# Performance work log

Measured on AMD Instinct MI355X. Metric: run time of the kernel, lower is better.

The kernel has to match this reference:

```python
import jax, jax.numpy as jnp
import numpy as np

N = 50000
E = 800000
F = 64
HID = 64
HEADS = 4
NTYPES = 3


def layer_norm(x, g, b, eps=1e-5):
    mu = x.mean(-1, keepdims=True)
    var = ((x - mu) ** 2).mean(-1, keepdims=True)
    return (x - mu) * jax.lax.rsqrt(var + eps) * g + b


def gat_conv(x, src, dst, n, W, att_src, att_dst, bias, concat):
    # PyG GATConv: per-head linear transform, additive attention, segment softmax over dst.
    H, C = att_src.shape
    xp = (x @ W).reshape(n, H, C)                       # [N,H,C]
    a_s = (xp * att_src).sum(-1)                         # [N,H]
    a_d = (xp * att_dst).sum(-1)                         # [N,H]
    e = jax.nn.leaky_relu(a_s[src] + a_d[dst], 0.2)      # [Etot,H]
    m = jax.ops.segment_max(e, dst, num_segments=n)      # stable softmax per target
    ex = jnp.exp(e - m[dst])
    denom = jax.ops.segment_sum(ex, dst, num_segments=n)
    alpha = ex / (denom[dst] + 1e-16)                    # [Etot,H]
    msg = xp[src] * alpha[:, :, None]                    # [Etot,H,C]
    out = jax.ops.segment_sum(msg, dst, num_segments=n)  # [N,H,C]
    out = out.reshape(n, H * C) if concat else out.mean(1)
    return out + bias


def setup_inputs() -> dict:
    key = jax.random.key(0)
    ks = jax.random.split(key, 12)
    f32 = jnp.float32
    return {
        'node_features': jax.random.normal(ks[0], (N, F), f32),
        'node_types': jax.random.randint(ks[1], (N,), 0, NTYPES),
        'edge_index': jax.random.randint(ks[2], (2, E), 0, N),
        'type_emb': jax.random.normal(ks[3], (NTYPES, HID), f32) * 0.02,
        'proj_W': jax.random.normal(ks[4], (F, HID), f32) / np.sqrt(F).astype(np.float32),
        'proj_b': jnp.zeros((HID,), f32),
        'W0': jax.random.normal(ks[5], (HID, HEADS * HID), f32) / np.sqrt(HID).astype(np.float32),
        'att_src0': jax.random.normal(ks[6], (HEADS, HID), f32) * 0.1,
        'att_dst0': jax.random.normal(ks[7], (HEADS, HID), f32) * 0.1,
        'bias0': jnp.zeros((HEADS * HID,), f32),
        'ln0_g': jnp.ones((HEADS * HID,), f32),
        'ln0_b': jnp.zeros((HEADS * HID,), f32),
        'W1': jax.random.normal(ks[8], (HEADS * HID, HEADS * HID), f32) / np.sqrt(HEADS * HID).astype(np.float32),
        'att_src1': jax.random.normal(ks[9], (HEADS, HID), f32) * 0.1,
        'att_dst1': jax.random.normal(ks[10], (HEADS, HID), f32) * 0.1,
        'bias1': jnp.zeros((HID,), f32),
        'ln1_g': jnp.ones((HID,), f32),
        'ln1_b': jnp.zeros((HID,), f32),
    }


def reference(node_features, node_types, edge_index, type_emb, proj_W, proj_b,
              W0, att_src0, att_dst0, bias0, ln0_g, ln0_b,
              W1, att_src1, att_dst1, bias1, ln1_g, ln1_b):
    n = node_features.shape[0]
    loop = jnp.arange(n)
    src = jnp.concatenate([edge_index[0], loop])  # add_self_loops=True (PyG default)
    dst = jnp.concatenate([edge_index[1], loop])
    # input projection + node-type embedding
    x = node_features @ proj_W + proj_b + type_emb[node_types]
    # layer 0: concat heads -> [N, HEADS*HID]
    h = gat_conv(x, src, dst, n, W0, att_src0, att_dst0, bias0, True)
    h = jax.nn.relu(layer_norm(h, ln0_g, ln0_b))  # dropout is identity in eval
    # layer 1: mean over heads -> [N, HID]; residual skipped (shape mismatch 256 vs 64)
    h2 = gat_conv(h, src, dst, n, W1, att_src1, att_dst1, bias1, False)
    h2 = jax.nn.relu(layer_norm(h2, ln1_g, ln1_b))
    return h2
```

## Files before the change

kernel.cpp:

```cpp
#include <hip/hip_runtime.h>
#include <hip/hip_bf16.h>
#include <hip/hip_fp16.h>

typedef unsigned short u16;
typedef unsigned int u32;
typedef short s16x8 __attribute__((ext_vector_type(8)));
typedef float f32x4 __attribute__((ext_vector_type(4)));

__device__ __forceinline__ float bf2f(u16 u) {
  return __uint_as_float(((u32)u) << 16);
}

__device__ __forceinline__ u16 f2b(float f) {
  __hip_bfloat16 h = __float2bfloat16(f);
  return *(u16*)&h;
}

__device__ __forceinline__ u32 packbf(float lo, float hi) {
  return (u32)f2b(lo) | ((u32)f2b(hi) << 16);
}

__device__ __forceinline__ bool sniff_bf16(const void* ones) {
  u32 w = *(const u32*)ones;
  return (w >> 16) == (w & 0xFFFFu);
}

__device__ __forceinline__ float ldf(const void* p, size_t i, bool bf) {
  return bf ? bf2f(((const u16*)p)[i]) : ((const float*)p)[i];
}

__global__ __launch_bounds__(256) void deg_count_k(const int* __restrict__ ei, int E, int N,
                                                   int* __restrict__ deg) {
  int i = blockIdx.x * 256 + threadIdx.x;
  if (i >= E + N) return;
  int d = (i < E) ? ei[E + i] : (i - E);
  atomicAdd(deg + d, 1);
}

__global__ __launch_bounds__(256) void scan_local_k(const int* __restrict__ deg,
                                                    int* __restrict__ off,
                                                    int* __restrict__ bsum, int N) {
  __shared__ int ps[256];
  int t = threadIdx.x;
  int i = blockIdx.x * 256 + t;
  int v = (i < N) ? deg[i] : 0;
  ps[t] = v;
  __syncthreads();
#pragma unroll
  for (int o = 1; o < 256; o <<= 1) {
    int u = (t >= o) ? ps[t - o] : 0;
    __syncthreads();
    ps[t] += u;
    __syncthreads();
  }
  if (i < N) off[i] = ps[t] - v;
  if (t == 255) bsum[blockIdx.x] = ps[255];
}

__global__ __launch_bounds__(256) void scan_add2_k(int* __restrict__ off,
                                                   const int* __restrict__ bsum,
                                                   int* __restrict__ cur,
                                                   int N, int Etot, int nb) {
  __shared__ int red[256];
  int t = threadIdx.x;
  int b = blockIdx.x;
  red[t] = (t < nb && t < b) ? bsum[t] : 0;
  __syncthreads();
#pragma unroll
  for (int o = 128; o > 0; o >>= 1) {
    if (t < o) red[t] += red[t + o];
    __syncthreads();
  }
  int pre = red[0];
  int i = b * 256 + t;
  if (i == 0) off[N] = Etot;
  if (i >= N) return;
  int o2 = off[i] + pre;
  off[i] = o2;
  cur[i] = o2;
}

__global__ __launch_bounds__(256) void scatter_k(const int* __restrict__ ei, int E, int N,
                                                 int* __restrict__ cur, int* __restrict__ csr) {
  int i = blockIdx.x * 256 + threadIdx.x;
  if (i >= E + N) return;
  int s, d;
  if (i < E) { s = ei[i]; d = ei[E + i]; } else { s = i - E; d = s; }
  int p = atomicAdd(cur + d, 1);
  csr[p] = s;
}

__global__ __launch_bounds__(256) void prep_k(
    const void* __restrict__ W0, const void* __restrict__ W1,
    const void* __restrict__ pW, const void* __restrict__ atts,
    const void* __restrict__ attd, const void* __restrict__ pb,
    const void* __restrict__ temb, const void* __restrict__ ones,
    u16* __restrict__ Wp0, u16* __restrict__ Wp1, u16* __restrict__ Wpp,
    u16* __restrict__ Wpe, float* __restrict__ ca) {
  bool bf = sniff_bf16(ones);
  int b = blockIdx.x;
  int t = threadIdx.x;
  if (b < 320) {
    const void* W = (b < 64) ? W0 : W1;
    u16* Wp = (b < 64) ? Wp0 : Wp1;
    int i = (b < 64 ? b : b - 64) * 256 + t;
    int j = i & 7;
    int q = (i >> 3) & 3;
    int c = (i >> 5) & 255;
    int kc = i >> 13;
    int k = kc * 32 + q * 8 + j;
    Wp[i] = f2b(ldf(W, (size_t)k * 256 + c, bf));
  } else if (b < 336) {
    int i = (b - 320) * 256 + t;
    int j = i & 7;
    int q = (i >> 3) & 3;
    int c = (i >> 5) & 63;
    int kc = i >> 11;
    int k = kc * 32 + q * 8 + j;
    Wpp[i] = f2b(ldf(pW, (size_t)k * 64 + c, bf));
  } else {
    __shared__ float va[256], vd[256];
    int h = t >> 6, k = t & 63;
    {
      float s = 0.f, d = 0.f;
      for (int c = 0; c < 64; c++) {
        float w = ldf(W0, (size_t)k * 256 + h * 64 + c, bf);
        s += w * ldf(atts, h * 64 + c, bf);
        d += w * ldf(attd, h * 64 + c, bf);
      }
      va[t] = s;
      vd[t] = d;
    }
    __syncthreads();
    {
      int i = k;
      float wa = 0.f, wd = 0.f;
      for (int kk = 0; kk < 64; kk++) {
        float wv = ldf(pW, (size_t)i * 64 + kk, bf);
        wa += wv * va[h * 64 + kk];
        wd += wv * vd[h * 64 + kk];
      }
      int kc = i >> 5, q = (i >> 3) & 3, j = i & 7;
      Wpe[((kc * 16 + h) * 4 + q) * 8 + j] = f2b(wa);
      Wpe[((kc * 16 + 4 + h) * 4 + q) * 8 + j] = f2b(wd);
    }
    Wpe[256 + t] = 0;
    Wpe[768 + t] = 0;
    if (t < 12) {
      int ty = t >> 2, hh = t & 3;
      float sa = 0.f, sd = 0.f;
      for (int kk = 0; kk < 64; kk++) {
        float bv = ldf(pb, kk, bf) + ldf(temb, ty * 64 + kk, bf);
        sa += bv * va[hh * 64 + kk];
        sd += bv * vd[hh * 64 + kk];
      }
      ca[t] = sa;
      ca[12 + t] = sd;
    }
  }
}

__global__ __launch_bounds__(256) void proj2_k(
    const void* __restrict__ nf, const int* __restrict__ ntype,
    const u16* __restrict__ Wpp, const u16* __restrict__ Wpe,
    const void* __restrict__ pbias, const void* __restrict__ temb,
    const float* __restrict__ ca, const void* __restrict__ ones,
    u16* __restrict__ x, float* __restrict__ aS, float* __restrict__ aD, int N) {
  bool bf = sniff_bf16(ones);
  int t = threadIdx.x;
  int wave = t >> 6, lane = t & 63;
  int r = lane & 15, q = lane >> 4;
  int row0 = blockIdx.x * 16;
  int arow = row0 + r;
  if (arow >= N) arow = N - 1;
  f32x4 xacc = {0.f, 0.f, 0.f, 0.f};
  f32x4 eacc = {0.f, 0.f, 0.f, 0.f};
#pragma unroll
  for (int kc = 0; kc < 2; kc++) {
    s16x8 a;
    if (bf) {
      a = *(const s16x8*)((const u16*)nf + (size_t)arow * 64 + kc * 32 + q * 8);
    } else {
      const float* fp = (const float*)nf + (size_t)arow * 64 + kc * 32 + q * 8;
#pragma unroll
      for (int j = 0; j < 8; j++) a[j] = (short)f2b(fp[j]);
    }
    {
      int c = wave * 16 + r;
      s16x8 b = *(const s16x8*)(Wpp + (((size_t)kc * 64 + c) * 4 + q) * 8);
      xacc = __builtin_amdgcn_mfma_f32_16x16x32_bf16(a, b, xacc, 0, 0, 0);
    }
    if (wave == 3) {
      s16x8 b = *(const s16x8*)(Wpe + (((size_t)kc * 16 + r) * 4 + q) * 8);
      eacc = __builtin_amdgcn_mfma_f32_16x16x32_bf16(a, b, eacc, 0, 0, 0);
    }
  }
#pragma unroll
  for (int rg = 0; rg < 4; rg++) {
    int row = row0 + q * 4 + rg;
    if (row >= N) continue;
    int col = wave * 16 + r;
    int ty = ntype[row];
    float v = xacc[rg] + ldf(pbias, col, bf) + ldf(temb, ty * 64 + col, bf);
    x[(size_t)row * 64 + col] = f2b(v);
    if (wave == 3 && r < 8) {
      if (r < 4) aS[(size_t)row * 4 + r] = eacc[rg] + ca[ty * 4 + r];
      else       aD[(size_t)row * 4 + (r - 4)] = eacc[rg] + ca[12 + ty * 4 + (r - 4)];
    }
  }
}

__global__ __launch_bounds__(256) void agg0_k(
    const int* __restrict__ off, const int* __restrict__ csr,
    const float* __restrict__ aS, const float* __restrict__ aD,
    const u16* __restrict__ x, u16* __restrict__ Ag, int N) {
  __shared__ float wlds[4][64][4];
  int wave = threadIdx.x >> 6;
  int lane = threadIdx.x & 63;
  int n = blockIdx.x * 4 + wave;
  if (n >= N) return;
  int start = off[n], end = off[n + 1];
  float4 ad4 = *(const float4*)(aD + (size_t)n * 4);
  float ad[4] = {ad4.x, ad4.y, ad4.z, ad4.w};
  float den[4] = {0.f, 0.f, 0.f, 0.f};
  int hv = lane >> 5;
  int cl = lane & 31;
  float accL[4] = {0.f, 0.f, 0.f, 0.f};
  float accH[4] = {0.f, 0.f, 0.f, 0.f};
  const char* wbase = (const char*)&wlds[wave][0][0] + hv * 16;
  u32 laneoff = (u32)cl * 4u;

  for (int cs = start; cs < end; cs += 64) {
    int cnt = end - cs; if (cnt > 64) cnt = 64;
    u32 sb = 0;
    float ex0 = 0.f, ex1 = 0.f, ex2 = 0.f, ex3 = 0.f;
    if (lane < cnt) {
      int s = csr[cs + lane];
      sb = (u32)s << 7;
      float4 as4 = *(const float4*)(aS + (size_t)s * 4);
      float v0 = as4.x + ad[0]; v0 = (v0 > 0.f ? v0 : 0.2f * v0) - 3.0f; ex0 = __expf(v0);
      float v1 = as4.y + ad[1]; v1 = (v1 > 0.f ? v1 : 0.2f * v1) - 3.0f; ex1 = __expf(v1);
      float v2 = as4.z + ad[2]; v2 = (v2 > 0.f ? v2 : 0.2f * v2) - 3.0f; ex2 = __expf(v2);
      float v3 = as4.w + ad[3]; v3 = (v3 > 0.f ? v3 : 0.2f * v3) - 3.0f; ex3 = __expf(v3);
      den[0] += ex0; den[1] += ex1; den[2] += ex2; den[3] += ex3;
    }
    *(float4*)&wlds[wave][lane][0] = make_float4(ex0, ex1, ex2, ex3);
    int cnt16 = (cnt + 15) & ~15;
    for (int e = 0; e < cnt16; e += 16) {
      u32 dd[8];
      float4 w[8];
#pragma unroll
      for (int j = 0; j < 8; j++) {
        u32 so0 = (u32)__builtin_amdgcn_readlane((int)sb, e + 2 * j);
        u32 so1 = (u32)__builtin_amdgcn_readlane((int)sb, e + 2 * j + 1);
        u32 so = hv ? so1 : so0;
        dd[j] = *(const u32*)((const char*)x + (so + laneoff));
      }
#pragma unroll
      for (int j = 0; j < 8; j++) {
        w[j] = *(const float4*)(wbase + (e + 2 * j) * 16);
      }
#pragma unroll
      for (int j = 0; j < 8; j++) {
        float xlo = __uint_as_float(dd[j] << 16);
        float xhi = __uint_as_float(dd[j] & 0xffff0000u);
        accL[0] += w[j].x * xlo; accH[0] += w[j].x * xhi;
        accL[1] += w[j].y * xlo; accH[1] += w[j].y * xhi;
        accL[2] += w[j].z * xlo; accH[2] += w[j].z * xhi;
        accL[3] += w[j].w * xlo; accH[3] += w[j].w * xhi;
      }
    }
  }
#pragma unroll
  for (int h = 0; h < 4; h++) {
#pragma unroll
    for (int o = 32; o > 0; o >>= 1) den[h] += __shfl_xor(den[h], o, 64);
  }
#pragma unroll
  for (int h = 0; h < 4; h++) {
    accL[h] += __shfl_xor(accL[h], 32, 64);
    accH[h] += __shfl_xor(accH[h], 32, 64);
  }
  if (lane < 32) {
    u32* agp = (u32*)Ag + (size_t)n * 128 + lane;
#pragma unroll
    for (int h = 0; h < 4; h++) {
      float inv = 1.f / (den[h] + 1e-16f);
      agp[h * 32] = packbf(accL[h] * inv, accH[h] * inv);
    }
  }
}

__global__ __launch_bounds__(256) void l0g1_k(
    const u16* __restrict__ Ag, const u16* __restrict__ Wp0,
    const void* __restrict__ bias0, const void* __restrict__ g0,
    const void* __restrict__ be0, const u16* __restrict__ Wp1,
    const void* __restrict__ atts, const void* __restrict__ attd,
    const void* __restrict__ ones,
    u16* __restrict__ C, float* __restrict__ aS, float* __restrict__ aD, int N) {
  bool bf = sniff_bf16(ones);
  __shared__ u16 hs[16][264];
  __shared__ float sm_s[4][16], sm_q[4][16];
  int t = threadIdx.x;
  int wave = t >> 6, lane = t & 63;
  int r = lane & 15, q = lane >> 4;
  int row0 = blockIdx.x * 16;
  int arow = row0 + r;
  if (arow >= N) arow = N - 1;
  {
    const u16* ap = Ag + (size_t)arow * 256 + wave * 64 + q * 8;
    f32x4 acc[4] = {{0.f, 0.f, 0.f, 0.f}, {0.f, 0.f, 0.f, 0.f},
                    {0.f, 0.f, 0.f, 0.f}, {0.f, 0.f, 0.f, 0.f}};
#pragma unroll
    for (int kc = 0; kc < 2; kc++) {
      s16x8 a = *(const s16x8*)(ap + kc * 32);
#pragma unroll
      for (int ct = 0; ct < 4; ct++) {
        int c = wave * 64 + ct * 16 + r;
        s16x8 b = *(const s16x8*)(Wp0 + (((size_t)kc * 256 + c) * 4 + q) * 8);
        acc[ct] = __builtin_amdgcn_mfma_f32_16x16x32_bf16(a, b, acc[ct], 0, 0, 0);
      }
    }
    float yv[4][4];
    float s_p[4] = {0.f, 0.f, 0.f, 0.f};
    float q_p[4] = {0.f, 0.f, 0.f, 0.f};
#pragma unroll
    for (int ct = 0; ct < 4; ct++) {
      float bc = ldf(bias0, wave * 64 + ct * 16 + r, bf);
#pragma unroll
      for (int rg = 0; rg < 4; rg++) {
        float y = acc[ct][rg] + bc;
        yv[ct][rg] = y;
        s_p[rg] += y;
        q_p[rg] += y * y;
      }
    }
#pragma unroll
    for (int o = 1; o < 16; o <<= 1) {
#pragma unroll
      for (int rg = 0; rg < 4; rg++) {
        s_p[rg] += __shfl_xor(s_p[rg], o, 64);
        q_p[rg] += __shfl_xor(q_p[rg], o, 64);
      }
    }
    if (r == 0) {
#pragma unroll
      for (int rg = 0; rg < 4; rg++) {
        sm_s[wave][q * 4 + rg] = s_p[rg];
        sm_q[wave][q * 4 + rg] = q_p[rg];
      }
    }
    __syncthreads();
#pragma unroll
    for (int rg = 0; rg < 4; rg++) {
      int lr = q * 4 + rg;
      float mu = (sm_s[0][lr] + sm_s[1][lr] + sm_s[2][lr] + sm_s[3][lr]) * (1.f / 256.f);
      float vq = (sm_q[0][lr] + sm_q[1][lr] + sm_q[2][lr] + sm_q[3][lr]) * (1.f / 256.f) - mu * mu;
      float inv = rsqrtf(vq + 1e-5f);
#pragma unroll
      for (int ct = 0; ct < 4; ct++) {
        int c = wave * 64 + ct * 16 + r;
        float o_ = (yv[ct][rg] - mu) * inv * ldf(g0, c, bf) + ldf(be0, c, bf);
        hs[lr][c] = f2b(fmaxf(o_, 0.f));
      }
    }
  }
  __syncthreads();
  int colw = wave * 64;
  f32x4 acc[4] = {{0.f, 0.f, 0.f, 0.f}, {0.f, 0.f, 0.f, 0.f},
                  {0.f, 0.f, 0.f, 0.f}, {0.f, 0.f, 0.f, 0.f}};
#pragma unroll
  for (int kc = 0; kc < 8; kc++) {
    s16x8 a = *(const s16x8*)&hs[r][kc * 32 + q * 8];
#pragma unroll
    for (int ct = 0; ct < 4; ct++) {
      int c = colw + ct * 16 + r;
      s16x8 b = *(const s16x8*)(Wp1 + (((size_t)kc * 256 + c) * 4 + q) * 8);
      acc[ct] = __builtin_amdgcn_mfma_f32_16x16x32_bf16(a, b, acc[ct], 0, 0, 0);
    }
  }
#pragma unroll
  for (int ct = 0; ct < 4; ct++) {
#pragma unroll
    for (int rg = 0; rg < 4; rg++) {
      int row = row0 + q * 4 + rg;
      if (row < N) C[(size_t)row * 256 + colw + ct * 16 + r] = f2b(acc[ct][rg]);
    }
  }
  float sp[4] = {0.f, 0.f, 0.f, 0.f};
  float dp[4] = {0.f, 0.f, 0.f, 0.f};
#pragma unroll
  for (int ct = 0; ct < 4; ct++) {
    int c = colw + ct * 16 + r;
    float av = ldf(atts, c, bf);
    float dv = ldf(attd, c, bf);
#pragma unroll
    for (int rg = 0; rg < 4; rg++) {
      sp[rg] += acc[ct][rg] * av;
      dp[rg] += acc[ct][rg] * dv;
    }
  }
#pragma unroll
  for (int o = 1; o < 16; o <<= 1) {
#pragma unroll
    for (int rg = 0; rg < 4; rg++) {
      sp[rg] += __shfl_xor(sp[rg], o, 64);
      dp[rg] += __shfl_xor(dp[rg], o, 64);
    }
  }
  if (r == 0) {
#pragma unroll
    for (int rg = 0; rg < 4; rg++) {
      int row = row0 + q * 4 + rg;
      if (row < N) {
        aS[(size_t)row * 4 + wave] = sp[rg];
        aD[(size_t)row * 4 + wave] = dp[rg];
      }
    }
  }
}

__global__ __launch_bounds__(256) void agg1_k(
    const int* __restrict__ off, const int* __restrict__ csr,
    const float* __restrict__ aS, const float* __restrict__ aD,
    const u16* __restrict__ xp,
    const void* __restrict__ bias, const void* __restrict__ g,
    const void* __restrict__ b, void* __restrict__ out, int N) {
  bool bf = sniff_bf16(g);
  __shared__ float wlds[4][64][4];
  int wave = threadIdx.x >> 6;
  int lane = threadIdx.x & 63;
  int n = blockIdx.x * 4 + wave;
  if (n >= N) return;
  int start = off[n], end = off[n + 1];
  float4 ad4 = *(const float4*)(aD + (size_t)n * 4);
  float ad[4] = {ad4.x, ad4.y, ad4.z, ad4.w};
  float den[4] = {0.f, 0.f, 0.f, 0.f};
  float acc[4] = {0.f, 0.f, 0.f, 0.f};
  int hh = lane >> 4;
  const float* wptr = &wlds[wave][0][0] + hh;
  u32 laneoff = (u32)lane * 8u;

  for (int cs = start; cs < end; cs += 64) {
    int cnt = end - cs; if (cnt > 64) cnt = 64;
    u32 sb = 0;
    float ex0 = 0.f, ex1 = 0.f, ex2 = 0.f, ex3 = 0.f;
    if (lane < cnt) {
      int s = csr[cs + lane];
      sb = (u32)s << 9;
      float4 as4 = *(const float4*)(aS + (size_t)s * 4);
      float v0 = as4.x + ad[0]; v0 = (v0 > 0.f ? v0 : 0.2f * v0) - 3.0f; ex0 = __expf(v0);
      float v1 = as4.y + ad[1]; v1 = (v1 > 0.f ? v1 : 0.2f * v1) - 3.0f; ex1 = __expf(v1);
      float v2 = as4.z + ad[2]; v2 = (v2 > 0.f ? v2 : 0.2f * v2) - 3.0f; ex2 = __expf(v2);
      float v3 = as4.w + ad[3]; v3 = (v3 > 0.f ? v3 : 0.2f * v3) - 3.0f; ex3 = __expf(v3);
      den[0] += ex0; den[1] += ex1; den[2] += ex2; den[3] += ex3;
    }
    *(float4*)&wlds[wave][lane][0] = make_float4(ex0, ex1, ex2, ex3);
    int cnt8 = (cnt + 7) & ~7;
    for (int e = 0; e < cnt8; e += 8) {
      uint2 d[8];
      float w[8];
#pragma unroll
      for (int j = 0; j < 8; j++) {
        u32 so = (u32)__builtin_amdgcn_readlane((int)sb, e + j);
        d[j] = *(const uint2*)((const char*)xp + (so + laneoff));
      }
#pragma unroll
      for (int j = 0; j < 8; j++) w[j] = wptr[(e + j) * 4];
#pragma unroll
      for (int j = 0; j < 8; j++) {
        acc[0] += w[j] * __uint_as_float(d[j].x << 16);
        acc[1] += w[j] * __uint_as_float(d[j].x & 0xffff0000u);
        acc[2] += w[j] * __uint_as_float(d[j].y << 16);
        acc[3] += w[j] * __uint_as_float(d[j].y & 0xffff0000u);
      }
    }
  }
#pragma unroll
  for (int h = 0; h < 4; h++) {
#pragma unroll
    for (int o = 32; o > 0; o >>= 1) den[h] += __shfl_xor(den[h], o, 64);
  }
  float dsel = (hh & 2) ? ((hh & 1) ? den[3] : den[2]) : ((hh & 1) ? den[1] : den[0]);
  float inv = 1.f / (dsel + 1e-16f);
  float p0 = acc[0] * inv, p1 = acc[1] * inv, p2 = acc[2] * inv, p3 = acc[3] * inv;
  p0 += __shfl_xor(p0, 16, 64); p0 += __shfl_xor(p0, 32, 64);
  p1 += __shfl_xor(p1, 16, 64); p1 += __shfl_xor(p1, 32, 64);
  p2 += __shfl_xor(p2, 16, 64); p2 += __shfl_xor(p2, 32, 64);
  p3 += __shfl_xor(p3, 16, 64); p3 += __shfl_xor(p3, 32, 64);
  int cb = (lane & 15) * 4;
  float z0 = 0.25f * p0 + ldf(bias, cb + 0, bf);
  float z1 = 0.25f * p1 + ldf(bias, cb + 1, bf);
  float z2 = 0.25f * p2 + ldf(bias, cb + 2, bf);
  float z3 = 0.25f * p3 + ldf(bias, cb + 3, bf);
  float sum = z0 + z1 + z2 + z3;
  sum += __shfl_xor(sum, 1, 64); sum += __shfl_xor(sum, 2, 64);
  sum += __shfl_xor(sum, 4, 64); sum += __shfl_xor(sum, 8, 64);
  float mu = sum * (1.f / 64.f);
  float d0 = z0 - mu, d1 = z1 - mu, d2 = z2 - mu, d3 = z3 - mu;
  float sq = d0 * d0 + d1 * d1 + d2 * d2 + d3 * d3;
  sq += __shfl_xor(sq, 1, 64); sq += __shfl_xor(sq, 2, 64);
  sq += __shfl_xor(sq, 4, 64); sq += __shfl_xor(sq, 8, 64);
  float invs = rsqrtf(sq * (1.f / 64.f) + 1e-5f);
  float y0 = fmaxf(d0 * invs * ldf(g, cb + 0, bf) + ldf(b, cb + 0, bf), 0.f);
  float y1 = fmaxf(d1 * invs * ldf(g, cb + 1, bf) + ldf(b, cb + 1, bf), 0.f);
  float y2 = fmaxf(d2 * invs * ldf(g, cb + 2, bf) + ldf(b, cb + 2, bf), 0.f);
  float y3 = fmaxf(d3 * invs * ldf(g, cb + 3, bf) + ldf(b, cb + 3, bf), 0.f);
  if (lane < 16) {
    if (bf) {
      u32* o32 = (u32*)out + (size_t)n * 32 + lane * 2;
      o32[0] = packbf(y0, y1);
      o32[1] = packbf(y2, y3);
    } else {
      ((float4*)out)[(size_t)n * 16 + lane] = make_float4(y0, y1, y2, y3);
    }
  }
}

extern "C" void kernel_launch(void* const* d_in, const int* in_sizes, int n_in,
                              void* d_out, int out_size, void* d_ws, size_t ws_size,
                              hipStream_t stream) {
  const void* nf   = d_in[0];
  const int* ntyp  = (const int*)d_in[1];
  const int* ei    = (const int*)d_in[2];
  const void* temb = d_in[3];
  const void* pW   = d_in[4];
  const void* pb   = d_in[5];
  const void* W0   = d_in[6];
  const void* as0  = d_in[7];
  const void* ad0  = d_in[8];
  const void* b0   = d_in[9];
  const void* g0   = d_in[10];
  const void* be0  = d_in[11];
  const void* W1   = d_in[12];
  const void* as1  = d_in[13];
  const void* ad1  = d_in[14];
  const void* b1   = d_in[15];
  const void* g1   = d_in[16];
  const void* be1  = d_in[17];

  int N = in_sizes[0] / 64;
  int E = in_sizes[2] / 2;
  int Etot = E + N;

  u16* Wp0 = (u16*)d_ws;
  u16* Wp1 = Wp0 + 64 * 256;
  u16* Wpp = Wp1 + 256 * 256;
  u16* Wpe = Wpp + 64 * 64;
  u16* xb  = Wpe + 1024;
  u16* Ag  = xb + (size_t)N * 64;
  u16* A   = Ag + (size_t)N * 256;
  float* aS0b = (float*)(A + (size_t)N * 256);
  float* aD0b = aS0b + (size_t)N * 4;
  float* aS1b = aD0b + (size_t)N * 4;
  float* aD1b = aS1b + (size_t)N * 4;
  float* ca = aD1b + (size_t)N * 4;
  int* deg  = (int*)(ca + 32);
  int* off  = deg + N;
  int* csr  = off + N + 1;
  int* bsum = csr + Etot;

  dim3 b256(256);
  int nodeBlocks = (N + 3) / 4;
  int edgeBlocksT = (Etot + 255) / 256;
  int gemmBlocks = (N + 15) / 16;
  int scanBlocks = (N + 255) / 256;

  hipMemsetAsync(deg, 0, (size_t)N * sizeof(int), stream);
  deg_count_k<<<edgeBlocksT, b256, 0, stream>>>(ei, E, N, deg);
  scan_local_k<<<scanBlocks, b256, 0, stream>>>(deg, off, bsum, N);
  scan_add2_k<<<scanBlocks, b256, 0, stream>>>(off, bsum, deg, N, Etot, scanBlocks);
  scatter_k<<<edgeBlocksT, b256, 0, stream>>>(ei, E, N, deg, csr);
  prep_k<<<337, b256, 0, stream>>>(W0, W1, pW, as0, ad0, pb, temb, g0,
                                   Wp0, Wp1, Wpp, Wpe, ca);

  proj2_k<<<gemmBlocks, b256, 0, stream>>>(nf, ntyp, Wpp, Wpe, pb, temb, ca, g0,
                                           xb, aS0b, aD0b, N);
  agg0_k<<<nodeBlocks, b256, 0, stream>>>(off, csr, aS0b, aD0b, xb, Ag, N);
  l0g1_k<<<gemmBlocks, b256, 0, stream>>>(Ag, Wp0, b0, g0, be0, Wp1, as1, ad1, g0,
                                          A, aS1b, aD1b, N);
  agg1_k<<<nodeBlocks, b256, 0, stream>>>(off, csr, aS1b, aD1b, A, b1, g1, be1, d_out, N);
}
```

Baseline: 393.0 us.

## Fold layer-1 attention vectors into weights and widen agg1 gather to 16 bytes

Precomputes W1·att_src1 and W1·att_dst1 into a small packed bf16 matrix in prep_k. l0g1_k then gets the per-head attention logits from one extra MFMA on wave 3, replacing the per-column dot products and shuffle reductions. Separately, agg1_k now gathers two edges per iteration with each half-wave loading 16 bytes (8 channels) per lane, which halves the number of gather instructions per edge; the halves are combined with cross-lane shuffles. Computing logits from bf16-rounded weights changes numerics slightly, and the wider gather uses more registers.

```diff
diff --git a/kernel.cpp b/kernel.cpp
--- a/kernel.cpp
+++ b/kernel.cpp
@@ -93,10 +93,11 @@
 __global__ __launch_bounds__(256) void prep_k(
     const void* __restrict__ W0, const void* __restrict__ W1,
     const void* __restrict__ pW, const void* __restrict__ atts,
-    const void* __restrict__ attd, const void* __restrict__ pb,
+    const void* __restrict__ attd, const void* __restrict__ as1,
+    const void* __restrict__ ad1, const void* __restrict__ pb,
     const void* __restrict__ temb, const void* __restrict__ ones,
     u16* __restrict__ Wp0, u16* __restrict__ Wp1, u16* __restrict__ Wpp,
-    u16* __restrict__ Wpe, float* __restrict__ ca) {
+    u16* __restrict__ Wpe, u16* __restrict__ Wpe1, float* __restrict__ ca) {
   bool bf = sniff_bf16(ones);
   int b = blockIdx.x;
   int t = threadIdx.x;
@@ -118,7 +119,7 @@
     int kc = i >> 11;
     int k = kc * 32 + q * 8 + j;
     Wpp[i] = f2b(ldf(pW, (size_t)k * 64 + c, bf));
-  } else {
+  } else if (b == 336) {
     __shared__ float va[256], vd[256];
     int h = t >> 6, k = t & 63;
     {
@@ -156,6 +157,28 @@
       }
       ca[t] = sa;
       ca[12 + t] = sd;
+    }
+  } else {
+    int k = t;
+    for (int z = t; z < 4096; z += 256) Wpe1[z] = 0;
+    __syncthreads();
+    float sa[4], sd[4];
+#pragma unroll
+    for (int h = 0; h < 4; h++) {
+      float a_ = 0.f, d_ = 0.f;
+      for (int j = 0; j < 64; j++) {
+        float wv = ldf(W1, (size_t)k * 256 + h * 64 + j, bf);
+        a_ += wv * ldf(as1, h * 64 + j, bf);
+        d_ += wv * ldf(ad1, h * 64 + j, bf);
+      }
+      sa[h] = a_;
+      sd[h] = d_;
+    }
+    int kc = k >> 5, q = (k >> 3) & 3, j = k & 7;
+#pragma unroll
+    for (int h = 0; h < 4; h++) {
+      Wpe1[((kc * 16 + h) * 4 + q) * 8 + j] = f2b(sa[h]);
+      Wpe1[((kc * 16 + 4 + h) * 4 + q) * 8 + j] = f2b(sd[h]);
     }
   }
 }
@@ -295,8 +318,7 @@
     const u16* __restrict__ Ag, const u16* __restrict__ Wp0,
     const void* __restrict__ bias0, const void* __restrict__ g0,
     const void* __restrict__ be0, const u16* __restrict__ Wp1,
-    const void* __restrict__ atts, const void* __restrict__ attd,
-    const void* __restrict__ ones,
+    const u16* __restrict__ Wpe1, const void* __restrict__ ones,
     u16* __restrict__ C, float* __restrict__ aS, float* __restrict__ aD, int N) {
   bool bf = sniff_bf16(ones);
   __shared__ u16 hs[16][264];
@@ -369,6 +391,7 @@
   int colw = wave * 64;
   f32x4 acc[4] = {{0.f, 0.f, 0.f, 0.f}, {0.f, 0.f, 0.f, 0.f},
                   {0.f, 0.f, 0.f, 0.f}, {0.f, 0.f, 0.f, 0.f}};
+  f32x4 eacc = {0.f, 0.f, 0.f, 0.f};
 #pragma unroll
   for (int kc = 0; kc < 8; kc++) {
     s16x8 a = *(const s16x8*)&hs[r][kc * 32 + q * 8];
@@ -378,6 +401,10 @@
       s16x8 b = *(const s16x8*)(Wp1 + (((size_t)kc * 256 + c) * 4 + q) * 8);
       acc[ct] = __builtin_amdgcn_mfma_f32_16x16x32_bf16(a, b, acc[ct], 0, 0, 0);
     }
+    if (wave == 3) {
+      s16x8 be = *(const s16x8*)(Wpe1 + (((size_t)kc * 16 + r) * 4 + q) * 8);
+      eacc = __builtin_amdgcn_mfma_f32_16x16x32_bf16(a, be, eacc, 0, 0, 0);
+    }
   }
 #pragma unroll
   for (int ct = 0; ct < 4; ct++) {
@@ -387,34 +414,13 @@
       if (row < N) C[(size_t)row * 256 + colw + ct * 16 + r] = f2b(acc[ct][rg]);
     }
   }
-  float sp[4] = {0.f, 0.f, 0.f, 0.f};
-  float dp[4] = {0.f, 0.f, 0.f, 0.f};
-#pragma unroll
-  for (int ct = 0; ct < 4; ct++) {
-    int c = colw + ct * 16 + r;
-    float av = ldf(atts, c, bf);
-    float dv = ldf(attd, c, bf);
-#pragma unroll
-    for (int rg = 0; rg < 4; rg++) {
-      sp[rg] += acc[ct][rg] * av;
-      dp[rg] += acc[ct][rg] * dv;
-    }
-  }
-#pragma unroll
-  for (int o = 1; o < 16; o <<= 1) {
-#pragma unroll
-    for (int rg = 0; rg < 4; rg++) {
-      sp[rg] += __shfl_xor(sp[rg], o, 64);
-      dp[rg] += __shfl_xor(dp[rg], o, 64);
-    }
-  }
-  if (r == 0) {
+  if (wave == 3 && r < 8) {
 #pragma unroll
     for (int rg = 0; rg < 4; rg++) {
       int row = row0 + q * 4 + rg;
       if (row < N) {
-        aS[(size_t)row * 4 + wave] = sp[rg];
-        aD[(size_t)row * 4 + wave] = dp[rg];
+        if (r < 4) aS[(size_t)row * 4 + r] = eacc[rg];
+        else       aD[(size_t)row * 4 + (r - 4)] = eacc[rg];
       }
     }
   }
@@ -436,10 +442,12 @@
   float4 ad4 = *(const float4*)(aD + (size_t)n * 4);
   float ad[4] = {ad4.x, ad4.y, ad4.z, ad4.w};
   float den[4] = {0.f, 0.f, 0.f, 0.f};
-  float acc[4] = {0.f, 0.f, 0.f, 0.f};
-  int hh = lane >> 4;
-  const float* wptr = &wlds[wave][0][0] + hh;
-  u32 laneoff = (u32)lane * 8u;
+  int l31 = lane & 31;
+  int eh = lane >> 5;
+  int head = l31 >> 3;
+  float acc[8] = {0.f, 0.f, 0.f, 0.f, 0.f, 0.f, 0.f, 0.f};
+  const float* wptr = &wlds[wave][0][0] + eh * 4 + head;
+  u32 laneoff = (u32)l31 * 16u;
 
   for (int cs = start; cs < end; cs += 64) {
     int cnt = end - cs; if (cnt > 64) cnt = 64;
@@ -456,23 +464,29 @@
       den[0] += ex0; den[1] += ex1; den[2] += ex2; den[3] += ex3;
     }
     *(float4*)&wlds[wave][lane][0] = make_float4(ex0, ex1, ex2, ex3);
-    int cnt8 = (cnt + 7) & ~7;
-    for (int e = 0; e < cnt8; e += 8) {
-      uint2 d[8];
+    int cnt16 = (cnt + 15) & ~15;
+    for (int e = 0; e < cnt16; e += 16) {
+      uint4 d[8];
       float w[8];
 #pragma unroll
       for (int j = 0; j < 8; j++) {
-        u32 so = (u32)__builtin_amdgcn_readlane((int)sb, e + j);
-        d[j] = *(const uint2*)((const char*)xp + (so + laneoff));
-      }
-#pragma unroll
-      for (int j = 0; j < 8; j++) w[j] = wptr[(e + j) * 4];
+        u32 so0 = (u32)__builtin_amdgcn_readlane((int)sb, e + 2 * j);
+        u32 so1 = (u32)__builtin_amdgcn_readlane((int)sb, e + 2 * j + 1);
+        u32 so = eh ? so1 : so0;
+        d[j] = *(const uint4*)((const char*)xp + (so + laneoff));
+      }
+#pragma unroll
+      for (int j = 0; j < 8; j++) w[j] = wptr[(e + 2 * j) * 4];
 #pragma unroll
       for (int j = 0; j < 8; j++) {
         acc[0] += w[j] * __uint_as_float(d[j].x << 16);
         acc[1] += w[j] * __uint_as_float(d[j].x & 0xffff0000u);
         acc[2] += w[j] * __uint_as_float(d[j].y << 16);
         acc[3] += w[j] * __uint_as_float(d[j].y & 0xffff0000u);
+        acc[4] += w[j] * __uint_as_float(d[j].z << 16);
+        acc[5] += w[j] * __uint_as_float(d[j].z & 0xffff0000u);
+        acc[6] += w[j] * __uint_as_float(d[j].w << 16);
+        acc[7] += w[j] * __uint_as_float(d[j].w & 0xffff0000u);
       }
     }
   }
@@ -481,38 +495,45 @@
 #pragma unroll
     for (int o = 32; o > 0; o >>= 1) den[h] += __shfl_xor(den[h], o, 64);
   }
-  float dsel = (hh & 2) ? ((hh & 1) ? den[3] : den[2]) : ((hh & 1) ? den[1] : den[0]);
+#pragma unroll
+  for (int j = 0; j < 8; j++) acc[j] += __shfl_xor(acc[j], 32, 64);
+  float dsel = (head & 2) ? ((head & 1) ? den[3] : den[2]) : ((head & 1) ? den[1] : den[0]);
   float inv = 1.f / (dsel + 1e-16f);
-  float p0 = acc[0] * inv, p1 = acc[1] * inv, p2 = acc[2] * inv, p3 = acc[3] * inv;
-  p0 += __shfl_xor(p0, 16, 64); p0 += __shfl_xor(p0, 32, 64);
-  p1 += __shfl_xor(p1, 16, 64); p1 += __shfl_xor(p1, 32, 64);
-  p2 += __shfl_xor(p2, 16, 64); p2 += __shfl_xor(p2, 32, 64);
-  p3 += __shfl_xor(p3, 16, 64); p3 += __shfl_xor(p3, 32, 64);
-  int cb = (lane & 15) * 4;
-  float z0 = 0.25f * p0 + ldf(bias, cb + 0, bf);
-  float z1 = 0.25f * p1 + ldf(bias, cb + 1, bf);
-  float z2 = 0.25f * p2 + ldf(bias, cb + 2, bf);
-  float z3 = 0.25f * p3 + ldf(bias, cb + 3, bf);
-  float sum = z0 + z1 + z2 + z3;
-  sum += __shfl_xor(sum, 1, 64); sum += __shfl_xor(sum, 2, 64);
-  sum += __shfl_xor(sum, 4, 64); sum += __shfl_xor(sum, 8, 64);
+#pragma unroll
+  for (int j = 0; j < 8; j++) {
+    float p = acc[j] * inv;
+    p += __shfl_xor(p, 8, 64);
+    p += __shfl_xor(p, 16, 64);
+    acc[j] = p;
+  }
+  int cb = lane & 7;
+  int c0 = cb * 8;
+  float z[8], y[8];
+  float sum = 0.f;
+#pragma unroll
+  for (int j = 0; j < 8; j++) {
+    z[j] = 0.25f * acc[j] + ldf(bias, c0 + j, bf);
+    sum += z[j];
+  }
+  sum += __shfl_xor(sum, 1, 64); sum += __shfl_xor(sum, 2, 64); sum += __shfl_xor(sum, 4, 64);
   float mu = sum * (1.f / 64.f);
-  float d0 = z0 - mu, d1 = z1 - mu, d2 = z2 - mu, d3 = z3 - mu;
-  float sq = d0 * d0 + d1 * d1 + d2 * d2 + d3 * d3;
-  sq += __shfl_xor(sq, 1, 64); sq += __shfl_xor(sq, 2, 64);
-  sq += __shfl_xor(sq, 4, 64); sq += __shfl_xor(sq, 8, 64);
+  float sq = 0.f;
+#pragma unroll
+  for (int j = 0; j < 8; j++) { z[j] -= mu; sq += z[j] * z[j]; }
+  sq += __shfl_xor(sq, 1, 64); sq += __shfl_xor(sq, 2, 64); sq += __shfl_xor(sq, 4, 64);
   float invs = rsqrtf(sq * (1.f / 64.f) + 1e-5f);
-  float y0 = fmaxf(d0 * invs * ldf(g, cb + 0, bf) + ldf(b, cb + 0, bf), 0.f);
-  float y1 = fmaxf(d1 * invs * ldf(g, cb + 1, bf) + ldf(b, cb + 1, bf), 0.f);
-  float y2 = fmaxf(d2 * invs * ldf(g, cb + 2, bf) + ldf(b, cb + 2, bf), 0.f);
-  float y3 = fmaxf(d3 * invs * ldf(g, cb + 3, bf) + ldf(b, cb + 3, bf), 0.f);
-  if (lane < 16) {
+#pragma unroll
+  for (int j = 0; j < 8; j++)
+    y[j] = fmaxf(z[j] * invs * ldf(g, c0 + j, bf) + ldf(b, c0 + j, bf), 0.f);
+  if (lane < 8) {
     if (bf) {
-      u32* o32 = (u32*)out + (size_t)n * 32 + lane * 2;
-      o32[0] = packbf(y0, y1);
-      o32[1] = packbf(y2, y3);
+      uint4 o4;
+      o4.x = packbf(y[0], y[1]); o4.y = packbf(y[2], y[3]);
+      o4.z = packbf(y[4], y[5]); o4.w = packbf(y[6], y[7]);
+      ((uint4*)out)[(size_t)n * 8 + cb] = o4;
     } else {
-      ((float4*)out)[(size_t)n * 16 + lane] = make_float4(y0, y1, y2, y3);
+      ((float4*)out)[(size_t)n * 16 + cb * 2] = make_float4(y[0], y[1], y[2], y[3]);
+      ((float4*)out)[(size_t)n * 16 + cb * 2 + 1] = make_float4(y[4], y[5], y[6], y[7]);
     }
   }
 }
@@ -547,7 +568,8 @@
   u16* Wp1 = Wp0 + 64 * 256;
   u16* Wpp = Wp1 + 256 * 256;
   u16* Wpe = Wpp + 64 * 64;
-  u16* xb  = Wpe + 1024;
+  u16* Wpe1 = Wpe + 1024;
+  u16* xb  = Wpe1 + 4096;
   u16* Ag  = xb + (size_t)N * 64;
   u16* A   = Ag + (size_t)N * 256;
   float* aS0b = (float*)(A + (size_t)N * 256);
@@ -571,13 +593,13 @@
   scan_local_k<<<scanBlocks, b256, 0, stream>>>(deg, off, bsum, N);
   scan_add2_k<<<scanBlocks, b256, 0, stream>>>(off, bsum, deg, N, Etot, scanBlocks);
   scatter_k<<<edgeBlocksT, b256, 0, stream>>>(ei, E, N, deg, csr);
-  prep_k<<<337, b256, 0, stream>>>(W0, W1, pW, as0, ad0, pb, temb, g0,
-                                   Wp0, Wp1, Wpp, Wpe, ca);
+  prep_k<<<338, b256, 0, stream>>>(W0, W1, pW, as0, ad0, as1, ad1, pb, temb, g0,
+                                   Wp0, Wp1, Wpp, Wpe, Wpe1, ca);
 
   proj2_k<<<gemmBlocks, b256, 0, stream>>>(nf, ntyp, Wpp, Wpe, pb, temb, ca, g0,
                                            xb, aS0b, aD0b, N);
   agg0_k<<<nodeBlocks, b256, 0, stream>>>(off, csr, aS0b, aD0b, xb, Ag, N);
-  l0g1_k<<<gemmBlocks, b256, 0, stream>>>(Ag, Wp0, b0, g0, be0, Wp1, as1, ad1, g0,
+  l0g1_k<<<gemmBlocks, b256, 0, stream>>>(Ag, Wp0, b0, g0, be0, Wp1, Wpe1, g0,
                                           A, aS1b, aD1b, N);
   agg1_k<<<nodeBlocks, b256, 0, stream>>>(off, csr, aS1b, aD1b, A, b1, g1, be1, d_out, N);
 }
```

Result: slower. 425.2 us (+8.2%).
